# Kernel tuning notes

Hardware: AMD Instinct MI355X
Metric: run time of the kernel (lower is better)

The kernel has to match this reference:

```python
import jax, jax.numpy as jnp
import numpy as np

BEAM = 4
START = 1


def setup_inputs() -> dict:
    key = jax.random.key(0)
    ks = jax.random.split(key, 10)
    S, B, H, E, V = 32, 16, 1024, 256, 32000
    Din = E + E + H  # embed + enc_input_step + enc_output_step
    sc = 0.02
    return {
        "enc_h_n": jax.random.normal(ks[0], (1, B, H), jnp.float32),
        "enc_c_n": jax.random.normal(ks[1], (1, B, H), jnp.float32),
        "enc_outputs": jax.random.normal(ks[2], (S, B, H), jnp.float32),
        "enc_inputs": jax.random.normal(ks[3], (S, B, E), jnp.float32),
        "embed": jax.random.normal(ks[4], (V, E), jnp.float32) * sc,
        "w_ih": jax.random.normal(ks[5], (Din, 4 * H), jnp.float32) * sc,
        "w_hh": jax.random.normal(ks[6], (H, 4 * H), jnp.float32) * sc,
        "b_lstm": jnp.zeros((4 * H,), jnp.float32),
        "w_out": jax.random.normal(ks[7], (H, V), jnp.float32) * sc,
        "b_out": jnp.zeros((V,), jnp.float32),
    }


def reference(enc_h_n, enc_c_n, enc_outputs, enc_inputs,
              embed, w_ih, w_hh, b_lstm, w_out, b_out):
    S, B, _ = enc_inputs.shape
    H = enc_h_n.shape[2]
    V = w_out.shape[1]
    K = BEAM

    def decode(word, h, c, ein, eout):
        # word: [B] int, h/c: [B,H], ein: [B,E], eout: [B,H]
        x = jnp.concatenate([embed[word], ein, eout], axis=-1)  # [B,Din]
        gates = x @ w_ih + h @ w_hh + b_lstm                    # [B,4H]
        i, f, g, o = jnp.split(gates, 4, axis=-1)
        c2 = jax.nn.sigmoid(f) * c + jax.nn.sigmoid(i) * jnp.tanh(g)
        h2 = jax.nn.sigmoid(o) * jnp.tanh(c2)
        logits = h2 @ w_out + b_out                             # [B,V]
        return logits, h2, c2

    # ---- init_beam_search (step 0) ----
    h0, c0 = enc_h_n[0], enc_c_n[0]
    word0 = jnp.full((B,), START, dtype=jnp.int32)
    logits0, h1, c1 = decode(word0, h0, c0, enc_inputs[0], enc_outputs[0])
    probs0 = jax.nn.softmax(logits0, axis=-1)
    top_v, top_i = jax.lax.top_k(probs0, K)  # [B,K]
    # NOTE: original code never updates current_scores inside the loop -> constant
    scores = top_v

    h = jnp.broadcast_to(h1, (K, B, H)) + 0.0  # per-beam hidden state copies
    c = jnp.broadcast_to(c1, (K, B, H)) + 0.0
    word = top_i  # [B,K]

    decode_beams = jax.vmap(decode, in_axes=(1, 0, 0, None, None))

    def step(carry, xs):
        h, c, word = carry
        ein, eout = xs
        logits, h2, c2 = decode_beams(word, h, c, ein, eout)  # [K,B,V]
        probs = jax.nn.softmax(logits, axis=-1)
        # space_search layout: beam b occupies cols [b*V, (b+1)*V); tile repeats
        # each beam score V times -> equivalent to broadcast over vocab axis.
        space = jnp.transpose(probs, (1, 0, 2)) * scores[:, :, None]  # [B,K,V]
        _, ti = jax.lax.top_k(space.reshape(B, K * V), K)             # [B,K]
        word2 = ti % V
        return (h2, c2, word2), ti

    (_, _, _), tis = jax.lax.scan(step, (h, c, word),
                                  (enc_inputs[1:], enc_outputs[1:]))
    out = jnp.concatenate([top_i[None], tis], axis=0)  # [S,B,K]
    return jnp.transpose(out, (2, 1, 0)).astype(jnp.int32)  # [K,B,S]
```

## Files before the change

### kernel.cpp

```cpp
#include <hip/hip_runtime.h>
#include <math.h>

#define S_LEN 32
#define B_N   16
#define H_N   1024
#define E_N   256
#define V_N   32000
#define KBEAM 4
#define DIN   1536
#define D2    2560
#define R_N   64
#define NDS   20
#define NB    500
#define LKS   2

typedef _Float16 f16;
typedef f16   f16x8 __attribute__((ext_vector_type(8)));
typedef float f32x4 __attribute__((ext_vector_type(4)));
#define MFMA(A,B,C) __builtin_amdgcn_mfma_f32_16x16x32_f16(A,B,C,0,0,0)

__device__ __forceinline__ float sigmf(float x){ return 1.0f/(1.0f+expf(-x)); }
__device__ __forceinline__ bool better(float v1,int i1,float v2,int i2){
  return (v1>v2) || (v1==v2 && i1<i2);
}
__device__ __forceinline__ void ins4(float bv,int bi,
    float&av0,float&av1,float&av2,float&av3,int&ai0,int&ai1,int&ai2,int&ai3){
  if (better(bv,bi,av3,ai3)){ av3=bv; ai3=bi;
    if (better(av3,ai3,av2,ai2)){ float t=av2;av2=av3;av3=t; int q=ai2;ai2=ai3;ai3=q;
      if (better(av2,ai2,av1,ai1)){ t=av1;av1=av2;av2=t; q=ai1;ai1=ai2;ai2=q;
        if (better(av1,ai1,av0,ai0)){ t=av0;av0=av1;av1=t; q=ai0;ai0=ai1;ai1=q; } } } }
}

#define FMA16(w4, h4) { \
  acc[0][0]=fmaf(w4.x,h4.x,acc[0][0]); acc[0][1]=fmaf(w4.x,h4.y,acc[0][1]); \
  acc[0][2]=fmaf(w4.x,h4.z,acc[0][2]); acc[0][3]=fmaf(w4.x,h4.w,acc[0][3]); \
  acc[1][0]=fmaf(w4.y,h4.x,acc[1][0]); acc[1][1]=fmaf(w4.y,h4.y,acc[1][1]); \
  acc[1][2]=fmaf(w4.y,h4.z,acc[1][2]); acc[1][3]=fmaf(w4.y,h4.w,acc[1][3]); \
  acc[2][0]=fmaf(w4.z,h4.x,acc[2][0]); acc[2][1]=fmaf(w4.z,h4.y,acc[2][1]); \
  acc[2][2]=fmaf(w4.z,h4.z,acc[2][2]); acc[2][3]=fmaf(w4.z,h4.w,acc[2][3]); \
  acc[3][0]=fmaf(w4.w,h4.x,acc[3][0]); acc[3][1]=fmaf(w4.w,h4.y,acc[3][1]); \
  acc[3][2]=fmaf(w4.w,h4.z,acc[3][2]); acc[3][3]=fmaf(w4.w,h4.w,acc[3][3]); }

__global__ __launch_bounds__(256) void k_init(
    const float* __restrict__ enc_h_n, const float* __restrict__ enc_c_n,
    const float* __restrict__ enc_outputs, const float* __restrict__ enc_inputs,
    const float* __restrict__ embed, float* __restrict__ x, float* __restrict__ c){
  int r = blockIdx.x, tid = threadIdx.x, b = r & 15;
  float* xr = x + (size_t)r*D2;
  xr[tid]        = embed[E_N + tid];
  xr[E_N + tid]  = enc_inputs[b*E_N + tid];
  #pragma unroll
  for (int q=0;q<4;++q) xr[2*E_N + q*256 + tid] = enc_outputs[b*H_N + q*256 + tid];
  #pragma unroll
  for (int q=0;q<4;++q) xr[DIN + q*256 + tid]   = enc_h_n[b*H_N + q*256 + tid];
  #pragma unroll
  for (int q=0;q<4;++q) c[(size_t)r*H_N + q*256 + tid] = enc_c_n[b*H_N + q*256 + tid];
}

__global__ __launch_bounds__(256) void k_convw(
    const float* __restrict__ w, f16* __restrict__ wpk){
  __shared__ f16 Th[64][66];
  __shared__ f16 Tl[64][66];
  int v0 = blockIdx.x*64, d0 = blockIdx.y*64;
  int tid = threadIdx.x;
  int r = tid >> 4, cq = (tid & 15)*4;
  #pragma unroll
  for (int rr=0; rr<4; ++rr){
    int d = r + rr*16;
    float4 x = *(const float4*)&w[(size_t)(d0+d)*V_N + v0 + cq];
    f16 h;
    h=(f16)x.x; Th[d][cq+0]=h; Tl[d][cq+0]=(f16)((x.x-(float)h)*4096.0f);
    h=(f16)x.y; Th[d][cq+1]=h; Tl[d][cq+1]=(f16)((x.y-(float)h)*4096.0f);
    h=(f16)x.z; Th[d][cq+2]=h; Tl[d][cq+2]=(f16)((x.z-(float)h)*4096.0f);
    h=(f16)x.w; Th[d][cq+3]=h; Tl[d][cq+3]=(f16)((x.w-(float)h)*4096.0f);
  }
  __syncthreads();
  int T2 = tid >> 6, l = tid & 63;
  int lm = l & 15, kq = l >> 4;
  int Tg = blockIdx.x*4 + T2;
  #pragma unroll
  for (int ks2=0; ks2<2; ++ks2){
    int ksg = blockIdx.y*2 + ks2;
    f16x8 a, b2;
    #pragma unroll
    for (int i=0;i<8;++i){
      int dd = ks2*32 + kq*8 + i;
      a[i]  = Th[dd][T2*16 + lm];
      b2[i] = Tl[dd][T2*16 + lm];
    }
    size_t base = ((size_t)(Tg*32 + ksg)*2)*512 + l*8;
    *(f16x8*)&wpk[base]       = a;
    *(f16x8*)&wpk[base + 512] = b2;
  }
}

#define GWLD(d, off) (*(const float4*)((((d) < DIN) ? (w_ih + (size_t)(d)*4096) \
                       : (w_hh + (size_t)((d)-DIN)*4096)) + (off)))
__global__ __launch_bounds__(256) void k_gates(
    const float* __restrict__ x, const float* __restrict__ w_ih,
    const float* __restrict__ w_hh, float* __restrict__ gpart){
  int tid = threadIdx.x;
  int jt = blockIdx.x, ks = blockIdx.y;
  int cx = tid & 15, ry = tid >> 4;
  int cb = jt*64;
  int wdd = tid >> 4, wseg = tid & 15;
  int xrow = tid >> 3, xseg = tid & 7;

  __shared__ float Wt0[32][64], Wt1[32][64];
  __shared__ float Xt0[32][68], Xt1[32][68];

  float acc[4][4];
  #pragma unroll
  for (int cc=0;cc<4;++cc)
    #pragma unroll
    for (int rr=0;rr<4;++rr) acc[cc][rr]=0.f;

  int d0 = ks*128;
  const float* xp0 = x + (size_t)xrow*D2 + d0 + xseg*4;
  const float* xp1 = x + (size_t)(xrow+32)*D2 + d0 + xseg*4;

#define GLQ(WA,WB,X0,X1, ch) { int d_ = d0 + (ch)*32; \
  WA = GWLD(d_+wdd,    cb+wseg*4); \
  WB = GWLD(d_+16+wdd, cb+wseg*4); \
  X0 = *(const float4*)(xp0 + (ch)*32); \
  X1 = *(const float4*)(xp1 + (ch)*32); }
#define GSQ(Wt,Xt, WA,WB,X0,X1) { \
  *(float4*)&Wt[wdd][wseg*4]    = WA; \
  *(float4*)&Wt[wdd+16][wseg*4] = WB; \
  Xt[xseg*4+0][xrow] = X0.x; Xt[xseg*4+1][xrow] = X0.y; \
  Xt[xseg*4+2][xrow] = X0.z; Xt[xseg*4+3][xrow] = X0.w; \
  Xt[xseg*4+0][xrow+32] = X1.x; Xt[xseg*4+1][xrow+32] = X1.y; \
  Xt[xseg*4+2][xrow+32] = X1.z; Xt[xseg*4+3][xrow+32] = X1.w; }
#define GCQ(Wt,Xt) { _Pragma("unroll 8") for (int dd=0; dd<32; ++dd){ \
    float4 w4 = *(const float4*)&Wt[dd][cx*4]; \
    float4 h4 = *(const float4*)&Xt[dd][ry*4]; \
    FMA16(w4, h4) } }

  float4 wA0,wB0,x00,x10, wA1,wB1,x01,x11;
  GLQ(wA0,wB0,x00,x10, 0)
  GSQ(Wt0,Xt0, wA0,wB0,x00,x10)
  GLQ(wA1,wB1,x01,x11, 1)
  __syncthreads();

  for (int ch=0; ch<4; ch+=2){
    if (ch+2<4) GLQ(wA0,wB0,x00,x10, ch+2)
    GSQ(Wt1,Xt1, wA1,wB1,x01,x11)
    GCQ(Wt0,Xt0)
    __syncthreads();
    if (ch+3<4) GLQ(wA1,wB1,x01,x11, ch+3)
    if (ch+2<4) GSQ(Wt0,Xt0, wA0,wB0,x00,x10)
    GCQ(Wt1,Xt1)
    if (ch+2<4) __syncthreads();
  }
  #pragma unroll
  for (int rr=0;rr<4;++rr){
    float4 o; o.x=acc[0][rr]; o.y=acc[1][rr]; o.z=acc[2][rr]; o.w=acc[3][rr];
    *(float4*)&gpart[((size_t)(ks*R_N + ry*4+rr))*4096 + cb + cx*4] = o;
  }
}

__global__ __launch_bounds__(256) void k_lstm(
    const float* __restrict__ gpart, const float* __restrict__ b_lstm,
    float* __restrict__ c, float* __restrict__ xn, float* __restrict__ h2t,
    f16* __restrict__ hpk){
  int r = blockIdx.x, tid = threadIdx.x;
  int j = blockIdx.y*256 + tid;
  float gi = b_lstm[j], gf = b_lstm[1024+j], gg = b_lstm[2048+j], go = b_lstm[3072+j];
  #pragma unroll
  for (int ds=0; ds<NDS; ++ds){
    size_t base = ((size_t)ds*R_N + r)*4096;
    gi += gpart[base + j];      gf += gpart[base + 1024 + j];
    gg += gpart[base + 2048+j]; go += gpart[base + 3072 + j];
  }
  float cv = c[(size_t)r*H_N + j];
  float c2 = sigmf(gf)*cv + sigmf(gi)*tanhf(gg);
  float h2 = sigmf(go)*tanhf(c2);
  c[(size_t)r*H_N + j] = c2;
  xn[(size_t)r*D2 + DIN + j] = h2;
  h2t[(size_t)j*R_N + r] = h2;
  f16 hh = (f16)h2;
  int m = r >> 4, lm = r & 15;
  int ks = j >> 5, kq = (j & 31) >> 3, i = j & 7;
  int l = lm + 16*kq;
  size_t base2 = ((size_t)(m*32 + ks)*2)*512 + l*8 + i;
  hpk[base2]       = hh;
  hpk[base2 + 512] = (f16)((h2 - (float)hh)*4096.0f);
}

__global__ __launch_bounds__(256) void k_logits_mfma(
    const f16* __restrict__ wpk, const f16* __restrict__ hpk,
    float* __restrict__ plog){
  int tid = threadIdx.x;
  int lane = tid & 63;
  int wv = tid >> 6;
  int T  = blockIdx.x*4 + wv;
  int vb = T*16;
  int ksb = blockIdx.y*16;

  const f16* wp  = wpk + ((size_t)(T*32 + ksb)*2)*512 + lane*8;
  const f16* hp0 = hpk + ((size_t)(0*32 + ksb)*2)*512 + lane*8;
  const f16* hp1 = hpk + ((size_t)(1*32 + ksb)*2)*512 + lane*8;
  const f16* hp2 = hpk + ((size_t)(2*32 + ksb)*2)*512 + lane*8;
  const f16* hp3 = hpk + ((size_t)(3*32 + ksb)*2)*512 + lane*8;

  f32x4 c10={0,0,0,0}, c11={0,0,0,0}, c12={0,0,0,0}, c13={0,0,0,0};
  f32x4 c20={0,0,0,0}, c21={0,0,0,0}, c22={0,0,0,0}, c23={0,0,0,0};

  f16x8 Bh0,Bl0,A0h0,A1h0,A2h0,A3h0,A0l0,A1l0,A2l0,A3l0;
  f16x8 Bh1,Bl1,A0h1,A1h1,A2h1,A3h1,A0l1,A1l1,A2l1,A3l1;

#define LOADSET(S, s) { size_t o_ = (size_t)(s)*1024; \
  Bh##S  = *(const f16x8*)(wp + o_);  Bl##S  = *(const f16x8*)(wp + o_ + 512); \
  A0h##S = *(const f16x8*)(hp0 + o_); A0l##S = *(const f16x8*)(hp0 + o_ + 512); \
  A1h##S = *(const f16x8*)(hp1 + o_); A1l##S = *(const f16x8*)(hp1 + o_ + 512); \
  A2h##S = *(const f16x8*)(hp2 + o_); A2l##S = *(const f16x8*)(hp2 + o_ + 512); \
  A3h##S = *(const f16x8*)(hp3 + o_); A3l##S = *(const f16x8*)(hp3 + o_ + 512); }
#define COMPSET(S) { \
  c10 = MFMA(A0h##S, Bh##S, c10); c20 = MFMA(A0l##S, Bh##S, c20); c20 = MFMA(A0h##S, Bl##S, c20); \
  c11 = MFMA(A1h##S, Bh##S, c11); c21 = MFMA(A1l##S, Bh##S, c21); c21 = MFMA(A1h##S, Bl##S, c21); \
  c12 = MFMA(A2h##S, Bh##S, c12); c22 = MFMA(A2l##S, Bh##S, c22); c22 = MFMA(A2h##S, Bl##S, c22); \
  c13 = MFMA(A3h##S, Bh##S, c13); c23 = MFMA(A3l##S, Bh##S, c23); c23 = MFMA(A3h##S, Bl##S, c23); }

  LOADSET(0, 0)
  for (int s=0; s<16; s+=2){
    LOADSET(1, s+1)
    COMPSET(0)
    if (s+2<16) LOADSET(0, s+2)
    COMPSET(1)
  }

  const float inv = 1.0f/4096.0f;
  int lm = lane & 15;
  int rb = (lane>>4)*4;
  size_t rbase = (size_t)blockIdx.y*R_N;
#define STT(mt, A1, A2) { \
  _Pragma("unroll") for (int rg=0; rg<4; ++rg){ \
    plog[(rbase + (mt)*16 + rb + rg)*(size_t)V_N + vb + lm] = A1[rg] + A2[rg]*inv; } }
  STT(0, c10, c20) STT(1, c11, c21) STT(2, c12, c22) STT(3, c13, c23)
}

__global__ __launch_bounds__(256) void k_stats(
    const float* __restrict__ plog, const float* __restrict__ b_out,
    float* __restrict__ pm, float* __restrict__ pz,
    float* __restrict__ pv, int* __restrict__ pi){
  int tid = threadIdx.x;
  int cx = tid & 15, ry = tid >> 4;
  int cb = blockIdx.x * 64;
  float4 bias = *(const float4*)&b_out[cb + cx*4];
  #pragma unroll
  for (int rr=0;rr<4;++rr){
    int row = ry*4 + rr;
    float4 a = *(const float4*)&plog[(size_t)row*V_N + cb + cx*4];
    float4 b2 = *(const float4*)&plog[(size_t)(R_N+row)*V_N + cb + cx*4];
    float v0 = a.x+b2.x+bias.x, v1 = a.y+b2.y+bias.y;
    float v2 = a.z+b2.z+bias.z, v3 = a.w+b2.w+bias.w;
    int   c0i = cb + cx*4;
    float tv0=-INFINITY,tv1=-INFINITY,tv2=-INFINITY,tv3=-INFINITY;
    int   ti0=0x7fffffff,ti1=0x7fffffff,ti2=0x7fffffff,ti3=0x7fffffff;
    ins4(v0,c0i+0,tv0,tv1,tv2,tv3,ti0,ti1,ti2,ti3);
    ins4(v1,c0i+1,tv0,tv1,tv2,tv3,ti0,ti1,ti2,ti3);
    ins4(v2,c0i+2,tv0,tv1,tv2,tv3,ti0,ti1,ti2,ti3);
    ins4(v3,c0i+3,tv0,tv1,tv2,tv3,ti0,ti1,ti2,ti3);
    float z = expf(v0-tv0)+expf(v1-tv0)+expf(v2-tv0)+expf(v3-tv0);
    #pragma unroll
    for (int msk=1; msk<16; msk<<=1){
      float om  = __shfl_xor(tv0, msk, 16);
      float oz  = __shfl_xor(z,   msk, 16);
      float ov1 = __shfl_xor(tv1, msk, 16);
      float ov2 = __shfl_xor(tv2, msk, 16);
      float ov3 = __shfl_xor(tv3, msk, 16);
      int   oi0 = __shfl_xor(ti0, msk, 16);
      int   oi1 = __shfl_xor(ti1, msk, 16);
      int   oi2 = __shfl_xor(ti2, msk, 16);
      int   oi3 = __shfl_xor(ti3, msk, 16);
      float M = fmaxf(tv0, om);
      z = z*expf(tv0-M) + oz*expf(om-M);
      ins4(om, oi0, tv0,tv1,tv2,tv3, ti0,ti1,ti2,ti3);
      ins4(ov1,oi1, tv0,tv1,tv2,tv3, ti0,ti1,ti2,ti3);
      ins4(ov2,oi2, tv0,tv1,tv2,tv3, ti0,ti1,ti2,ti3);
      ins4(ov3,oi3, tv0,tv1,tv2,tv3, ti0,ti1,ti2,ti3);
    }
    if (cx == 0){
      size_t base = (size_t)row*NB + blockIdx.x;
      pm[base]=tv0; pz[base]=z;
      pv[base*4+0]=tv0; pv[base*4+1]=tv1; pv[base*4+2]=tv2; pv[base*4+3]=tv3;
      pi[base*4+0]=ti0; pi[base*4+1]=ti1; pi[base*4+2]=ti2; pi[base*4+3]=ti3;
    }
  }
}

__global__ __launch_bounds__(256) void k_logits_fused(
    const float* __restrict__ h2t, const float* __restrict__ w_out,
    const float* __restrict__ b_out,
    float* __restrict__ pm, float* __restrict__ pz,
    float* __restrict__ pv, int* __restrict__ pi){
  int tid = threadIdx.x;
  int cx  = tid & 15, ry = tid >> 4;
  int cb  = blockIdx.x * 64;
  int sdd = tid >> 4, seg = tid & 15;
  __shared__ float Wt[32][64];
  __shared__ float Ht[32][64];
  float acc[4][4];
  #pragma unroll
  for (int cc=0;cc<4;++cc)
    #pragma unroll
    for (int rr=0;rr<4;++rr) acc[cc][rr]=0.f;
  const float* gW = w_out + (size_t)sdd*V_N + cb + seg*4;
  const float* gH = h2t + sdd*64 + seg*4;
#define FLQ(WA,WB,HA,HB, ch) { \
  const float* gWn = gW + (size_t)(ch)*32*V_N; \
  const float* gHn = gH + (size_t)(ch)*32*64; \
  WA = *(const float4*)gWn; WB = *(const float4*)(gWn + (size_t)16*V_N); \
  HA = *(const float4*)gHn; HB = *(const float4*)(gHn + 16*64); }
#define FSQ(WA,WB,HA,HB) { \
  *(float4*)&Wt[sdd][seg*4]    = WA; \
  *(float4*)&Wt[sdd+16][seg*4] = WB; \
  *(float4*)&Ht[sdd][seg*4]    = HA; \
  *(float4*)&Ht[sdd+16][seg*4] = HB; }
#define FCQ() { _Pragma("unroll 8") for (int dd=0; dd<32; ++dd){ \
    float4 w4 = *(const float4*)&Wt[dd][cx*4]; \
    float4 h4 = *(const float4*)&Ht[dd][ry*4]; \
    FMA16(w4, h4) } }
  float4 wA0,wB0,hA0,hB0, wA1,wB1,hA1,hB1;
  FLQ(wA0,wB0,hA0,hB0, 0)
  FSQ(wA0,wB0,hA0,hB0)
  FLQ(wA1,wB1,hA1,hB1, 1)
  __syncthreads();
  for (int ch=0; ch<32; ch+=2){
    if (ch+2<32) FLQ(wA0,wB0,hA0,hB0, ch+2)
    FCQ()
    __syncthreads();
    FSQ(wA1,wB1,hA1,hB1)
    __syncthreads();
    if (ch+3<32) FLQ(wA1,wB1,hA1,hB1, ch+3)
    FCQ()
    if (ch+2<32){
      __syncthreads();
      FSQ(wA0,wB0,hA0,hB0)
      __syncthreads();
    }
  }
  float4 bias = *(const float4*)&b_out[cb + cx*4];
  #pragma unroll
  for (int rr=0;rr<4;++rr){
    float v0 = acc[0][rr]+bias.x, v1 = acc[1][rr]+bias.y;
    float v2 = acc[2][rr]+bias.z, v3 = acc[3][rr]+bias.w;
    int   c0i = cb + cx*4;
    float tv0=-INFINITY,tv1=-INFINITY,tv2=-INFINITY,tv3=-INFINITY;
    int   ti0=0x7fffffff,ti1=0x7fffffff,ti2=0x7fffffff,ti3=0x7fffffff;
    ins4(v0,c0i+0,tv0,tv1,tv2,tv3,ti0,ti1,ti2,ti3);
    ins4(v1,c0i+1,tv0,tv1,tv2,tv3,ti0,ti1,ti2,ti3);
    ins4(v2,c0i+2,tv0,tv1,tv2,tv3,ti0,ti1,ti2,ti3);
    ins4(v3,c0i+3,tv0,tv1,tv2,tv3,ti0,ti1,ti2,ti3);
    float z = expf(v0-tv0)+expf(v1-tv0)+expf(v2-tv0)+expf(v3-tv0);
    #pragma unroll
    for (int msk=1; msk<16; msk<<=1){
      float om  = __shfl_xor(tv0, msk, 16);
      float oz  = __shfl_xor(z,   msk, 16);
      float ov1 = __shfl_xor(tv1, msk, 16);
      float ov2 = __shfl_xor(tv2, msk, 16);
      float ov3 = __shfl_xor(tv3, msk, 16);
      int   oi0 = __shfl_xor(ti0, msk, 16);
      int   oi1 = __shfl_xor(ti1, msk, 16);
      int   oi2 = __shfl_xor(ti2, msk, 16);
      int   oi3 = __shfl_xor(ti3, msk, 16);
      float M = fmaxf(tv0, om);
      z = z*expf(tv0-M) + oz*expf(om-M);
      ins4(om, oi0, tv0,tv1,tv2,tv3, ti0,ti1,ti2,ti3);
      ins4(ov1,oi1, tv0,tv1,tv2,tv3, ti0,ti1,ti2,ti3);
      ins4(ov2,oi2, tv0,tv1,tv2,tv3, ti0,ti1,ti2,ti3);
      ins4(ov3,oi3, tv0,tv1,tv2,tv3, ti0,ti1,ti2,ti3);
    }
    if (cx == 0){
      int row = ry*4 + rr;
      size_t base = (size_t)row*NB + blockIdx.x;
      pm[base]=tv0; pz[base]=z;
      pv[base*4+0]=tv0; pv[base*4+1]=tv1; pv[base*4+2]=tv2; pv[base*4+3]=tv3;
      pi[base*4+0]=ti0; pi[base*4+1]=ti1; pi[base*4+2]=ti2; pi[base*4+3]=ti3;
    }
  }
}

__global__ __launch_bounds__(256) void k_final(
    const float* __restrict__ pm, const float* __restrict__ pz,
    const float* __restrict__ pv, const int* __restrict__ pi,
    float* __restrict__ scores, int* __restrict__ out, int t,
    float* __restrict__ xn,
    const float* __restrict__ enc_inputs, const float* __restrict__ enc_outputs,
    const float* __restrict__ embed){
  int b = blockIdx.x, tid = threadIdx.x;
  int kk = tid >> 6, lane = tid & 63;
  __shared__ float fM[KBEAM], fZ[KBEAM], fV[16];
  __shared__ int   fI[16], sw[KBEAM];
  int nk = (t==0) ? 1 : KBEAM;
  if (kk < nk){
    size_t rb = (size_t)(kk*B_N + b)*NB;
    float m=-INFINITY, z=0.f;
    float av0=-INFINITY,av1=-INFINITY,av2=-INFINITY,av3=-INFINITY;
    int   ai0=0x7fffffff,ai1=0x7fffffff,ai2=0x7fffffff,ai3=0x7fffffff;
    for (int p0=lane; p0<NB; p0+=64){
      size_t p = rb + p0;
      float mf = pm[p];
      float M = fmaxf(m, mf);
      z = z*expf(m-M) + pz[p]*expf(mf-M);
      m = M;
      #pragma unroll
      for (int q=0;q<4;++q)
        ins4(pv[p*4+q], pi[p*4+q], av0,av1,av2,av3, ai0,ai1,ai2,ai3);
    }
    #pragma unroll
    for (int msk=1; msk<64; msk<<=1){
      float om  = __shfl_xor(m,   msk);
      float oz  = __shfl_xor(z,   msk);
      float ov0 = __shfl_xor(av0, msk);
      float ov1 = __shfl_xor(av1, msk);
      float ov2 = __shfl_xor(av2, msk);
      float ov3 = __shfl_xor(av3, msk);
      int   oi0 = __shfl_xor(ai0, msk);
      int   oi1 = __shfl_xor(ai1, msk);
      int   oi2 = __shfl_xor(ai2, msk);
      int   oi3 = __shfl_xor(ai3, msk);
      float M = fmaxf(m, om);
      z = z*expf(m-M) + oz*expf(om-M);
      m = M;
      ins4(ov0,oi0, av0,av1,av2,av3, ai0,ai1,ai2,ai3);
      ins4(ov1,oi1, av0,av1,av2,av3, ai0,ai1,ai2,ai3);
      ins4(ov2,oi2, av0,av1,av2,av3, ai0,ai1,ai2,ai3);
      ins4(ov3,oi3, av0,av1,av2,av3, ai0,ai1,ai2,ai3);
    }
    if (lane == 0){
      fM[kk]=m; fZ[kk]=z;
      fV[kk*4+0]=av0; fV[kk*4+1]=av1; fV[kk*4+2]=av2; fV[kk*4+3]=av3;
      fI[kk*4+0]=ai0; fI[kk*4+1]=ai1; fI[kk*4+2]=ai2; fI[kk*4+3]=ai3;
    }
  }
  __syncthreads();
  if (tid==0){
    if (t==0){
      #pragma unroll
      for (int j=0;j<4;++j){
        float p = expf(fV[j]-fM[0])/fZ[0];
        scores[b*4+j] = p;
        out[j*(B_N*S_LEN) + b*S_LEN] = fI[j];
        sw[j] = fI[j];
      }
    } else {
      float cv[16]; int cj[16];
      for (int k=0;k<4;++k){
        float s = scores[b*4+k];
        #pragma unroll
        for (int j=0;j<4;++j){
          cv[k*4+j] = expf(fV[k*4+j]-fM[k])/fZ[k]*s;
          cj[k*4+j] = k*V_N + fI[k*4+j];
        }
      }
      bool used[16];
      for (int i=0;i<16;++i) used[i]=false;
      for (int rank=0;rank<4;++rank){
        int best=-1;
        for (int i=0;i<16;++i){
          if (used[i]) continue;
          if (best<0 || cv[i]>cv[best] || (cv[i]==cv[best] && cj[i]<cj[best])) best=i;
        }
        used[best]=true;
        out[rank*(B_N*S_LEN) + b*S_LEN + t] = cj[best];
        sw[rank] = cj[best] % V_N;
      }
    }
  }
  __syncthreads();
  if (t < S_LEN-1){
    const float* ein = enc_inputs  + (size_t)(t+1)*B_N*E_N + (size_t)b*E_N;
    const float* eo  = enc_outputs + (size_t)(t+1)*B_N*H_N + (size_t)b*H_N;
    #pragma unroll
    for (int j=0;j<KBEAM;++j){
      float* xr = xn + (size_t)(j*B_N + b)*D2;
      const float* em = embed + (size_t)sw[j]*E_N;
      xr[tid]       = em[tid];
      xr[E_N + tid] = ein[tid];
      #pragma unroll
      for (int q=0;q<4;++q) xr[2*E_N + q*256 + tid] = eo[q*256 + tid];
    }
  }
}

extern "C" void kernel_launch(void* const* d_in, const int* in_sizes, int n_in,
                              void* d_out, int out_size, void* d_ws, size_t ws_size,
                              hipStream_t stream) {
  (void)in_sizes; (void)n_in; (void)out_size;
  const float* enc_h_n     = (const float*)d_in[0];
  const float* enc_c_n     = (const float*)d_in[1];
  const float* enc_outputs = (const float*)d_in[2];
  const float* enc_inputs  = (const float*)d_in[3];
  const float* embed       = (const float*)d_in[4];
  const float* w_ih        = (const float*)d_in[5];
  const float* w_hh        = (const float*)d_in[6];
  const float* b_lstm      = (const float*)d_in[7];
  const float* w_out       = (const float*)d_in[8];
  const float* b_out       = (const float*)d_in[9];
  int* out = (int*)d_out;

  float* ws = (float*)d_ws;
  const size_t FRONTF = (size_t)R_N*D2*2 + (size_t)R_N*H_N + (size_t)H_N*R_N;
  const size_t HSPLF  = (size_t)R_N*H_N;
  const size_t PLOGF  = (size_t)LKS*R_N*V_N;
  const size_t GPARTF = (size_t)NDS*R_N*4096;
  const size_t STATF  = (size_t)R_N*NB*10;
  const size_t WSPLF  = (size_t)V_N*H_N;
  size_t bigF = (PLOGF > GPARTF ? PLOGF : GPARTF);
  size_t need_split = (FRONTF + HSPLF + bigF + STATF + 64 + WSPLF)*sizeof(float);
  bool use_split = (ws_size >= need_split);

  float* xA     = ws;
  float* xB     = xA + (size_t)R_N*D2;
  float* cbuf   = xB + (size_t)R_N*D2;
  float* h2t    = cbuf + (size_t)R_N*H_N;
  f16*   hpk    = (f16*)(h2t + (size_t)H_N*R_N);
  float* big    = h2t + (size_t)H_N*R_N + HSPLF;
  float* gpart  = big;
  float* plog   = big;
  float* pm     = big + bigF;
  float* pz     = pm + (size_t)R_N*NB;
  float* pv     = pz + (size_t)R_N*NB;
  int*   pi     = (int*)(pv + (size_t)R_N*NB*4);
  float* scoresb= (float*)(pi + (size_t)R_N*NB*4);
  f16*   wpk    = (f16*)(scoresb + 64);

  if (use_split){
    k_convw<<<dim3(V_N/64, H_N/64), 256, 0, stream>>>(w_out, wpk);
  }
  k_init<<<R_N, 256, 0, stream>>>(enc_h_n, enc_c_n, enc_outputs, enc_inputs, embed, xA, cbuf);

  for (int t=0; t<S_LEN; ++t){
    float* xc = (t & 1) ? xB : xA;
    float* xn = (t & 1) ? xA : xB;
    k_gates <<<dim3(64, NDS), 256, 0, stream>>>(xc, w_ih, w_hh, gpart);
    k_lstm  <<<dim3(R_N, 4), 256, 0, stream>>>(gpart, b_lstm, cbuf, xn, h2t, hpk);
    if (use_split){
      k_logits_mfma<<<dim3(V_N/64, LKS), 256, 0, stream>>>(wpk, hpk, plog);
      k_stats<<<NB, 256, 0, stream>>>(plog, b_out, pm, pz, pv, pi);
    } else {
      k_logits_fused<<<NB, 256, 0, stream>>>(h2t, w_out, b_out, pm, pz, pv, pi);
    }
    k_final <<<B_N, 256, 0, stream>>>(pm, pz, pv, pi, scoresb, out, t, xn,
                                      enc_inputs, enc_outputs, embed);
  }
}
```

Measured before the change: 3.109 ms.

## Fuse logits MFMA with per-block softmax/top-k stats via shared memory

Removes the two-way K split of the logits GEMM and the separate stats kernel. Each block now runs the full K=1024 reduction, adds the bias, stages its 64x64 logits tile in LDS, and computes the per-block max, sum and top-4 directly. This drops the plog round trip through global memory and one launch per step. The cost is half as many blocks (500 instead of 1000) with twice the serial K loop each, which lowers parallelism for the GEMM.

```diff
diff --git a/kernel.cpp b/kernel.cpp
--- a/kernel.cpp
+++ b/kernel.cpp
@@ -12,7 +12,6 @@
 #define R_N   64
 #define NDS   20
 #define NB    500
-#define LKS   2
 
 typedef _Float16 f16;
 typedef f16   f16x8 __attribute__((ext_vector_type(8)));
@@ -189,19 +188,20 @@
 
 __global__ __launch_bounds__(256) void k_logits_mfma(
     const f16* __restrict__ wpk, const f16* __restrict__ hpk,
-    float* __restrict__ plog){
+    const float* __restrict__ b_out,
+    float* __restrict__ pm, float* __restrict__ pz,
+    float* __restrict__ pv, int* __restrict__ pi){
   int tid = threadIdx.x;
   int lane = tid & 63;
   int wv = tid >> 6;
   int T  = blockIdx.x*4 + wv;
   int vb = T*16;
-  int ksb = blockIdx.y*16;
-
-  const f16* wp  = wpk + ((size_t)(T*32 + ksb)*2)*512 + lane*8;
-  const f16* hp0 = hpk + ((size_t)(0*32 + ksb)*2)*512 + lane*8;
-  const f16* hp1 = hpk + ((size_t)(1*32 + ksb)*2)*512 + lane*8;
-  const f16* hp2 = hpk + ((size_t)(2*32 + ksb)*2)*512 + lane*8;
-  const f16* hp3 = hpk + ((size_t)(3*32 + ksb)*2)*512 + lane*8;
+
+  const f16* wp  = wpk + ((size_t)(T*32))*2*512 + lane*8;
+  const f16* hp0 = hpk + ((size_t)(0*32))*2*512 + lane*8;
+  const f16* hp1 = hpk + ((size_t)(1*32))*2*512 + lane*8;
+  const f16* hp2 = hpk + ((size_t)(2*32))*2*512 + lane*8;
+  const f16* hp3 = hpk + ((size_t)(3*32))*2*512 + lane*8;
 
   f32x4 c10={0,0,0,0}, c11={0,0,0,0}, c12={0,0,0,0}, c13={0,0,0,0};
   f32x4 c20={0,0,0,0}, c21={0,0,0,0}, c22={0,0,0,0}, c23={0,0,0,0};
@@ -222,38 +222,32 @@
   c13 = MFMA(A3h##S, Bh##S, c13); c23 = MFMA(A3l##S, Bh##S, c23); c23 = MFMA(A3h##S, Bl##S, c23); }
 
   LOADSET(0, 0)
-  for (int s=0; s<16; s+=2){
+  for (int s=0; s<32; s+=2){
     LOADSET(1, s+1)
     COMPSET(0)
-    if (s+2<16) LOADSET(0, s+2)
+    if (s+2<32) LOADSET(0, s+2)
     COMPSET(1)
   }
+
+  __shared__ float Ls[64][68];
 
   const float inv = 1.0f/4096.0f;
   int lm = lane & 15;
   int rb = (lane>>4)*4;
-  size_t rbase = (size_t)blockIdx.y*R_N;
+  float bias = b_out[vb + lm];
 #define STT(mt, A1, A2) { \
   _Pragma("unroll") for (int rg=0; rg<4; ++rg){ \
-    plog[(rbase + (mt)*16 + rb + rg)*(size_t)V_N + vb + lm] = A1[rg] + A2[rg]*inv; } }
+    Ls[(mt)*16 + rb + rg][wv*16 + lm] = A1[rg] + A2[rg]*inv + bias; } }
   STT(0, c10, c20) STT(1, c11, c21) STT(2, c12, c22) STT(3, c13, c23)
-}
-
-__global__ __launch_bounds__(256) void k_stats(
-    const float* __restrict__ plog, const float* __restrict__ b_out,
-    float* __restrict__ pm, float* __restrict__ pz,
-    float* __restrict__ pv, int* __restrict__ pi){
-  int tid = threadIdx.x;
+  __syncthreads();
+
   int cx = tid & 15, ry = tid >> 4;
   int cb = blockIdx.x * 64;
-  float4 bias = *(const float4*)&b_out[cb + cx*4];
   #pragma unroll
   for (int rr=0;rr<4;++rr){
     int row = ry*4 + rr;
-    float4 a = *(const float4*)&plog[(size_t)row*V_N + cb + cx*4];
-    float4 b2 = *(const float4*)&plog[(size_t)(R_N+row)*V_N + cb + cx*4];
-    float v0 = a.x+b2.x+bias.x, v1 = a.y+b2.y+bias.y;
-    float v2 = a.z+b2.z+bias.z, v3 = a.w+b2.w+bias.w;
+    float v0 = Ls[row][cx*4+0], v1 = Ls[row][cx*4+1];
+    float v2 = Ls[row][cx*4+2], v3 = Ls[row][cx*4+3];
     int   c0i = cb + cx*4;
     float tv0=-INFINITY,tv1=-INFINITY,tv2=-INFINITY,tv3=-INFINITY;
     int   ti0=0x7fffffff,ti1=0x7fffffff,ti2=0x7fffffff,ti3=0x7fffffff;
@@ -503,12 +497,10 @@
   float* ws = (float*)d_ws;
   const size_t FRONTF = (size_t)R_N*D2*2 + (size_t)R_N*H_N + (size_t)H_N*R_N;
   const size_t HSPLF  = (size_t)R_N*H_N;
-  const size_t PLOGF  = (size_t)LKS*R_N*V_N;
   const size_t GPARTF = (size_t)NDS*R_N*4096;
   const size_t STATF  = (size_t)R_N*NB*10;
   const size_t WSPLF  = (size_t)V_N*H_N;
-  size_t bigF = (PLOGF > GPARTF ? PLOGF : GPARTF);
-  size_t need_split = (FRONTF + HSPLF + bigF + STATF + 64 + WSPLF)*sizeof(float);
+  size_t need_split = (FRONTF + HSPLF + GPARTF + STATF + 64 + WSPLF)*sizeof(float);
   bool use_split = (ws_size >= need_split);
 
   float* xA     = ws;
@@ -518,8 +510,7 @@
   f16*   hpk    = (f16*)(h2t + (size_t)H_N*R_N);
   float* big    = h2t + (size_t)H_N*R_N + HSPLF;
   float* gpart  = big;
-  float* plog   = big;
-  float* pm     = big + bigF;
+  float* pm     = big + GPARTF;
   float* pz     = pm + (size_t)R_N*NB;
   float* pv     = pz + (size_t)R_N*NB;
   int*   pi     = (int*)(pv + (size_t)R_N*NB*4);
@@ -537,8 +528,7 @@
     k_gates <<<dim3(64, NDS), 256, 0, stream>>>(xc, w_ih, w_hh, gpart);
     k_lstm  <<<dim3(R_N, 4), 256, 0, stream>>>(gpart, b_lstm, cbuf, xn, h2t, hpk);
     if (use_split){
-      k_logits_mfma<<<dim3(V_N/64, LKS), 256, 0, stream>>>(wpk, hpk, plog);
-      k_stats<<<NB, 256, 0, stream>>>(plog, b_out, pm, pz, pv, pi);
+      k_logits_mfma<<<NB, 256, 0, stream>>>(wpk, hpk, b_out, pm, pz, pv, pi);
     } else {
       k_logits_fused<<<NB, 256, 0, stream>>>(h2t, w_out, b_out, pm, pz, pv, pi);
     }
```

Measured after the change: 2.852 ms. 1.09x faster.
